# Kernel tuning notes

Measured on AMD Instinct MI355X. Metric: run time of the kernel, lower is better.

The kernel has to match this reference:

```python
import jax, jax.numpy as jnp
import numpy as np

B, S, D = 2, 2048, 1024
H, DH = 16, 64
INNER = H * DH  # 1024
FF = 4 * D
WINDOW = 128
EPS = 1e-5
SCALE = DH ** -0.5


def setup_inputs() -> dict:
    key = jax.random.key(0)
    ks = jax.random.split(key, 8)
    s = lambda fan_in: 1.0 / np.sqrt(fan_in)
    return {
        "x": jax.random.normal(ks[0], (B, S, D), dtype=jnp.float32),
        "ln1_g": jnp.ones((D,), jnp.float32),
        "ln1_b": jnp.zeros((D,), jnp.float32),
        "w_qkv": jax.random.uniform(ks[1], (3 * INNER, D), jnp.float32, -s(D), s(D)),
        "w_out": jax.random.uniform(ks[2], (D, INNER), jnp.float32, -s(INNER), s(INNER)),
        "b_out": jnp.zeros((D,), jnp.float32),
        "ln2_g": jnp.ones((D,), jnp.float32),
        "ln2_b": jnp.zeros((D,), jnp.float32),
        "w_ff1": jax.random.uniform(ks[3], (FF, D), jnp.float32, -s(D), s(D)),
        "b_ff1": jnp.zeros((FF,), jnp.float32),
        "w_ff2": jax.random.uniform(ks[4], (D, FF), jnp.float32, -s(FF), s(FF)),
        "b_ff2": jnp.zeros((D,), jnp.float32),
    }


def _layernorm(x, g, b):
    mu = jnp.mean(x, axis=-1, keepdims=True)
    var = jnp.mean(jnp.square(x - mu), axis=-1, keepdims=True)
    return (x - mu) * jax.lax.rsqrt(var + EPS) * g + b


def reference(x, ln1_g, ln1_b, w_qkv, w_out, b_out, ln2_g, ln2_b, w_ff1, b_ff1, w_ff2, b_ff2):
    # --- attention block ---
    residual = x
    h = _layernorm(x, ln1_g, ln1_b)
    qkv = h @ w_qkv.T                             # [B, S, 3*INNER]
    q, k, v = jnp.split(qkv, 3, axis=-1)
    reshape_heads = lambda t: t.reshape(B, S, H, DH).transpose(0, 2, 1, 3)  # [B,H,S,DH]
    q, k, v = map(reshape_heads, (q, k, v))
    q = q * SCALE
    scores = jnp.einsum("bhqd,bhkd->bhqk", q, k)  # dense [B,H,S,S]
    # local sparse pattern: attend iff |i-j| <= window_size
    idx = jnp.arange(S)
    local_mask = jnp.abs(idx[:, None] - idx[None, :]) <= WINDOW  # [S,S] bool
    scores = jnp.where(local_mask[None, None], scores, -jnp.inf)
    attn = jax.nn.softmax(scores, axis=-1)
    attn = jnp.nan_to_num(attn, nan=0.0)
    out = jnp.einsum("bhqk,bhkd->bhqd", attn, v)  # [B,H,S,DH]
    out = out.transpose(0, 2, 1, 3).reshape(B, S, INNER)
    out = out @ w_out.T + b_out                   # dropout inactive (eval)
    x = residual + out
    # --- FFN block ---
    residual = x
    h = _layernorm(x, ln2_g, ln2_b)
    h = jax.nn.gelu(h @ w_ff1.T + b_ff1, approximate=False)
    h = h @ w_ff2.T + b_ff2
    return residual + h
```

## Files before the change

### kernel.cpp

```cpp
#include <hip/hip_runtime.h>
#include <stdint.h>

#define SEQ    2048
#define NB     2
#define DMODEL 1024
#define NHEAD  16
#define HDIM   64
#define FFDIM  4096
#define WIN    128
#define MTOK   (NB*SEQ)

typedef short short8 __attribute__((ext_vector_type(8)));
typedef float f32x4  __attribute__((ext_vector_type(4)));

__device__ __forceinline__ float bf2f(uint16_t h){ return __uint_as_float(((uint32_t)h) << 16); }
__device__ __forceinline__ uint16_t f2bf(float f){
  uint32_t u = __float_as_uint(f);
  u += 0x7fffu + ((u >> 16) & 1u);
  return (uint16_t)(u >> 16);
}

__device__ __forceinline__ float gelu_f(float v){
  float u = 0.7978845608028654f * v * (1.0f + 0.044715f * v * v);
  u = fminf(fmaxf(u, -10.0f), 10.0f);
  const float e = __expf(2.0f * u);
  const float th = (e - 1.0f) / (e + 1.0f);
  return 0.5f * v * (1.0f + th);
}

__device__ __forceinline__ void gl_lds16(const void* g, void* l) {
  __builtin_amdgcn_global_load_lds((const __attribute__((address_space(1))) void*)g,
                                   (__attribute__((address_space(3))) void*)l, 16, 0, 0);
}

__global__ __launch_bounds__(256) void cvtln_kernel(
    const float* __restrict__ s0, const float* __restrict__ s1,
    const float* __restrict__ s2, const float* __restrict__ s3,
    uint16_t* __restrict__ d0, uint16_t* __restrict__ d1,
    uint16_t* __restrict__ d2, uint16_t* __restrict__ d3,
    const float* __restrict__ x, const float* __restrict__ g,
    const float* __restrict__ b, uint16_t* __restrict__ y)
{
  __shared__ float red[8];
  const int t = threadIdx.x;
  if (blockIdx.x < 12288) {
    size_t i = (size_t)blockIdx.x * 256 + t;
    const float* s; uint16_t* d; size_t off;
    if      (i <  768*1024) { s = s0; d = d0; off = i; }
    else if (i < 1024*1024) { s = s1; d = d1; off = i -  768*1024; }
    else if (i < 2048*1024) { s = s2; d = d2; off = i - 1024*1024; }
    else                    { s = s3; d = d3; off = i - 2048*1024; }
    const float4 v = ((const float4*)s)[off];
    uint2 o;
    o.x = (uint32_t)f2bf(v.x) | ((uint32_t)f2bf(v.y) << 16);
    o.y = (uint32_t)f2bf(v.z) | ((uint32_t)f2bf(v.w) << 16);
    ((uint2*)d)[off] = o;
  } else {
    const int row = blockIdx.x - 12288;
    const float4 v = ((const float4*)(x + (size_t)row * DMODEL))[t];
    float s1 = v.x + v.y + v.z + v.w;
    float s2 = v.x*v.x + v.y*v.y + v.z*v.z + v.w*v.w;
    #pragma unroll
    for (int off = 32; off; off >>= 1) { s1 += __shfl_xor(s1, off, 64); s2 += __shfl_xor(s2, off, 64); }
    const int w = t >> 6;
    if ((t & 63) == 0) { red[w] = s1; red[4+w] = s2; }
    __syncthreads();
    s1 = red[0]+red[1]+red[2]+red[3];
    s2 = red[4]+red[5]+red[6]+red[7];
    const float mu = s1 * (1.0f/DMODEL);
    const float var = s2 * (1.0f/DMODEL) - mu*mu;
    const float rs = rsqrtf(var + 1e-5f);
    const float4 gv = ((const float4*)g)[t];
    const float4 bv = ((const float4*)b)[t];
    uint2 o;
    o.x = (uint32_t)f2bf((v.x-mu)*rs*gv.x + bv.x) | ((uint32_t)f2bf((v.y-mu)*rs*gv.y + bv.y) << 16);
    o.y = (uint32_t)f2bf((v.z-mu)*rs*gv.z + bv.z) | ((uint32_t)f2bf((v.w-mu)*rs*gv.w + bv.w) << 16);
    ((uint2*)(y + (size_t)row * DMODEL))[t] = o;
  }
}

__global__ __launch_bounds__(256) void ln_kernel(const float* __restrict__ x,
                                                 const float* __restrict__ g,
                                                 const float* __restrict__ b,
                                                 uint16_t* __restrict__ y)
{
  const int row = blockIdx.x;
  const int t = threadIdx.x;
  const float4 v = ((const float4*)(x + (size_t)row * DMODEL))[t];
  float s1 = v.x + v.y + v.z + v.w;
  float s2 = v.x*v.x + v.y*v.y + v.z*v.z + v.w*v.w;
  #pragma unroll
  for (int off = 32; off; off >>= 1) { s1 += __shfl_xor(s1, off, 64); s2 += __shfl_xor(s2, off, 64); }
  __shared__ float red[8];
  const int w = t >> 6;
  if ((t & 63) == 0) { red[w] = s1; red[4+w] = s2; }
  __syncthreads();
  s1 = red[0]+red[1]+red[2]+red[3];
  s2 = red[4]+red[5]+red[6]+red[7];
  const float mu = s1 * (1.0f/DMODEL);
  const float var = s2 * (1.0f/DMODEL) - mu*mu;
  const float rs = rsqrtf(var + 1e-5f);
  const float4 gv = ((const float4*)g)[t];
  const float4 bv = ((const float4*)b)[t];
  uint2 o;
  o.x = (uint32_t)f2bf((v.x-mu)*rs*gv.x + bv.x) | ((uint32_t)f2bf((v.y-mu)*rs*gv.y + bv.y) << 16);
  o.y = (uint32_t)f2bf((v.z-mu)*rs*gv.z + bv.z) | ((uint32_t)f2bf((v.w-mu)*rs*gv.w + bv.w) << 16);
  ((uint2*)(y + (size_t)row * DMODEL))[t] = o;
}


template<int EPI>
__global__ __launch_bounds__(256) void gemm_bt(
    const uint16_t* __restrict__ A, const uint16_t* __restrict__ Bm,
    const float* __restrict__ bias, uint16_t* __restrict__ C,
    int M, int N, int K)
{
  __shared__ __align__(16) uint16_t As[128*64];
  __shared__ __align__(16) uint16_t Bs[128*64];
  const int t = threadIdx.x;
  const int l = t & 63;
  const int w = t >> 6;
  const int row0 = blockIdx.y * 128;
  const int col0 = blockIdx.x * 128;
  const int wm = (w >> 1) * 64, wn = (w & 1) * 64;

  f32x4 acc[4][4];
  #pragma unroll
  for (int i = 0; i < 4; ++i)
    #pragma unroll
    for (int j = 0; j < 4; ++j)
      #pragma unroll
      for (int e = 0; e < 4; ++e) acc[i][j][e] = 0.0f;

  const int sr8 = t >> 3;
  const int sg  = (t & 7) ^ (sr8 & 7);
  const uint16_t* aG = A  + (size_t)(row0 + sr8) * K + sg * 8;
  const uint16_t* bG = Bm + (size_t)(col0 + sr8) * K + sg * 8;
  char* aL = (char*)As + t * 16;
  char* bL = (char*)Bs + t * 16;
  const int mrow = l & 15;
  const int kq = l >> 4;

  for (int k0 = 0; k0 < K; k0 += 64) {
    #pragma unroll
    for (int c = 0; c < 4; ++c) {
      gl_lds16(aG + k0 + (size_t)(c*32) * K, aL + c*4096);
      gl_lds16(bG + k0 + (size_t)(c*32) * K, bL + c*4096);
    }
    __syncthreads();
    #pragma unroll
    for (int ks = 0; ks < 2; ++ks) {
      const int pa = ((ks*4 + kq) ^ (mrow & 7)) * 16;
      short8 af[4], bfr[4];
      #pragma unroll
      for (int mi = 0; mi < 4; ++mi)
        af[mi] = *(const short8*)((const char*)As + (wm + mi*16 + mrow) * 128 + pa);
      #pragma unroll
      for (int ni = 0; ni < 4; ++ni)
        bfr[ni] = *(const short8*)((const char*)Bs + (wn + ni*16 + mrow) * 128 + pa);
      #pragma unroll
      for (int mi = 0; mi < 4; ++mi)
        #pragma unroll
        for (int ni = 0; ni < 4; ++ni)
          acc[mi][ni] = __builtin_amdgcn_mfma_f32_16x16x32_bf16(af[mi], bfr[ni], acc[mi][ni], 0, 0, 0);
    }
    __syncthreads();
  }

  const int crow = (l >> 4) * 4;
  float bv[4];
  #pragma unroll
  for (int ni = 0; ni < 4; ++ni)
    bv[ni] = (EPI != 0) ? bias[col0 + wn + ni*16 + mrow] : 0.0f;
  #pragma unroll
  for (int mi = 0; mi < 4; ++mi) {
    #pragma unroll
    for (int r = 0; r < 4; ++r) {
      const int row = row0 + wm + mi*16 + crow + r;
      #pragma unroll
      for (int ni = 0; ni < 4; ++ni) {
        const int col = col0 + wn + ni*16 + mrow;
        float v = acc[mi][ni][r] + bv[ni];
        if (EPI == 2) v = gelu_f(v);
        C[(size_t)row * N + col] = f2bf(v);
      }
    }
  }
}

__global__ __launch_bounds__(256) void gemm_qkv(
    const uint16_t* __restrict__ A, const uint16_t* __restrict__ Bm,
    uint16_t* __restrict__ C, int M, int N, int K)
{
  __shared__ __align__(16) uint16_t As[128*64];
  __shared__ __align__(16) uint16_t Bs[64*64];
  const int t = threadIdx.x;
  const int l = t & 63;
  const int w = t >> 6;
  const int row0 = blockIdx.y * 128;
  const int col0 = blockIdx.x * 64;
  const int wm = (w >> 1) * 64, wn = (w & 1) * 32;

  f32x4 acc[4][2];
  #pragma unroll
  for (int i = 0; i < 4; ++i)
    #pragma unroll
    for (int j = 0; j < 2; ++j)
      #pragma unroll
      for (int e = 0; e < 4; ++e) acc[i][j][e] = 0.0f;

  const int sr8 = t >> 3;
  const int sg  = (t & 7) ^ (sr8 & 7);
  const uint16_t* aG = A  + (size_t)(row0 + sr8) * K + sg * 8;
  const uint16_t* bG = Bm + (size_t)(col0 + sr8) * K + sg * 8;
  char* aL = (char*)As + t * 16;
  char* bL = (char*)Bs + t * 16;
  const int mrow = l & 15;
  const int kq = l >> 4;

  for (int k0 = 0; k0 < K; k0 += 64) {
    #pragma unroll
    for (int c = 0; c < 4; ++c)
      gl_lds16(aG + k0 + (size_t)(c*32) * K, aL + c*4096);
    #pragma unroll
    for (int c = 0; c < 2; ++c)
      gl_lds16(bG + k0 + (size_t)(c*32) * K, bL + c*4096);
    __syncthreads();
    #pragma unroll
    for (int ks = 0; ks < 2; ++ks) {
      const int pa = ((ks*4 + kq) ^ (mrow & 7)) * 16;
      short8 af[4], bfr[2];
      #pragma unroll
      for (int mi = 0; mi < 4; ++mi)
        af[mi] = *(const short8*)((const char*)As + (wm + mi*16 + mrow) * 128 + pa);
      #pragma unroll
      for (int ni = 0; ni < 2; ++ni)
        bfr[ni] = *(const short8*)((const char*)Bs + (wn + ni*16 + mrow) * 128 + pa);
      #pragma unroll
      for (int mi = 0; mi < 4; ++mi)
        #pragma unroll
        for (int ni = 0; ni < 2; ++ni)
          acc[mi][ni] = __builtin_amdgcn_mfma_f32_16x16x32_bf16(af[mi], bfr[ni], acc[mi][ni], 0, 0, 0);
    }
    __syncthreads();
  }

  const int crow = (l >> 4) * 4;
  #pragma unroll
  for (int mi = 0; mi < 4; ++mi)
    #pragma unroll
    for (int r = 0; r < 4; ++r) {
      const int row = row0 + wm + mi*16 + crow + r;
      #pragma unroll
      for (int ni = 0; ni < 2; ++ni)
        C[(size_t)row * N + col0 + wn + ni*16 + mrow] = f2bf(acc[mi][ni][r]);
    }
}

__global__ __launch_bounds__(256) void gemm64(
    const uint16_t* __restrict__ A, const uint16_t* __restrict__ Bm,
    const float* __restrict__ bias, const float* __restrict__ res,
    float* __restrict__ out, int M, int N, int K)
{
  __shared__ __align__(16) uint16_t As[64*64];
  __shared__ __align__(16) uint16_t Bs[64*64];
  const int t = threadIdx.x;
  const int l = t & 63;
  const int w = t >> 6;
  const int row0 = blockIdx.y * 64;
  const int col0 = blockIdx.x * 64;
  const int wm = (w >> 1) * 32, wn = (w & 1) * 32;

  f32x4 acc[2][2];
  #pragma unroll
  for (int i = 0; i < 2; ++i)
    #pragma unroll
    for (int j = 0; j < 2; ++j)
      #pragma unroll
      for (int e = 0; e < 4; ++e) acc[i][j][e] = 0.0f;

  const int sr8 = t >> 3;
  const int sg  = (t & 7) ^ (sr8 & 7);
  const uint16_t* aG = A  + (size_t)(row0 + sr8) * K + sg * 8;
  const uint16_t* bG = Bm + (size_t)(col0 + sr8) * K + sg * 8;
  char* aL = (char*)As + t * 16;
  char* bL = (char*)Bs + t * 16;
  const int mrow = l & 15;
  const int kq = l >> 4;

  for (int k0 = 0; k0 < K; k0 += 64) {
    gl_lds16(aG + k0,                    aL);
    gl_lds16(aG + k0 + (size_t)32 * K,   aL + 4096);
    gl_lds16(bG + k0,                    bL);
    gl_lds16(bG + k0 + (size_t)32 * K,   bL + 4096);
    __syncthreads();
    #pragma unroll
    for (int ks = 0; ks < 2; ++ks) {
      const int pa = ((ks*4 + kq) ^ (mrow & 7)) * 16;
      short8 af[2], bfr[2];
      #pragma unroll
      for (int mi = 0; mi < 2; ++mi)
        af[mi] = *(const short8*)((const char*)As + (wm + mi*16 + mrow) * 128 + pa);
      #pragma unroll
      for (int ni = 0; ni < 2; ++ni)
        bfr[ni] = *(const short8*)((const char*)Bs + (wn + ni*16 + mrow) * 128 + pa);
      #pragma unroll
      for (int mi = 0; mi < 2; ++mi)
        #pragma unroll
        for (int ni = 0; ni < 2; ++ni)
          acc[mi][ni] = __builtin_amdgcn_mfma_f32_16x16x32_bf16(af[mi], bfr[ni], acc[mi][ni], 0, 0, 0);
    }
    __syncthreads();
  }

  const int crow = (l >> 4) * 4;
  float bv[2];
  #pragma unroll
  for (int ni = 0; ni < 2; ++ni)
    bv[ni] = bias[col0 + wn + ni*16 + mrow];
  #pragma unroll
  for (int mi = 0; mi < 2; ++mi)
    #pragma unroll
    for (int r = 0; r < 4; ++r) {
      const int row = row0 + wm + mi*16 + crow + r;
      #pragma unroll
      for (int ni = 0; ni < 2; ++ni) {
        const int col = col0 + wn + ni*16 + mrow;
        out[(size_t)row * N + col] = acc[mi][ni][r] + bv[ni] + res[(size_t)row * N + col];
      }
    }
}

#define TQ    32
#define NKT   18
#define NKP   (NKT*16)
#define KSTR  72
#define PSTR  296

__global__ __launch_bounds__(256) void attn_kernel(const uint16_t* __restrict__ qkv,
                                                   uint16_t* __restrict__ out)
{
  __shared__ uint16_t Qs[TQ * KSTR];
  __shared__ uint16_t Ps[TQ * PSTR];
  __shared__ uint16_t KV[NKP * KSTR];
  const int t = threadIdx.x, l = t & 63, w = t >> 6;
  const int b = blockIdx.z, hh = blockIdx.y, q0 = blockIdx.x * TQ;
  const int k0 = (q0 - WIN > 0) ? (q0 - WIN) : 0;
  const int kend_ = q0 + TQ + WIN;
  const int kend = (kend_ < SEQ) ? kend_ : SEQ;
  const int nk = kend - k0;

  {
    const int r = t >> 3, gg = t & 7;
    const uint4 qv = *(const uint4*)(qkv + (size_t)(b*SEQ + q0 + r) * 3072 + hh*64 + gg*8);
    *(uint4*)((char*)Qs + r*(KSTR*2) + gg*16) = qv;
    for (int j = r; j < NKP; j += 32) {
      uint4 kv; kv.x = 0; kv.y = 0; kv.z = 0; kv.w = 0;
      if (j < nk)
        kv = *(const uint4*)(qkv + (size_t)(b*SEQ + k0 + j) * 3072 + 1024 + hh*64 + gg*8);
      *(uint4*)((char*)KV + j*(KSTR*2) + gg*16) = kv;
    }
  }
  __syncthreads();

  if (w < 2) {
    const int rb = w * 16;
    const int mrow = l & 15, q4 = l >> 4;
    const short8 aq0 = *(const short8*)((const char*)Qs + (rb + mrow)*(KSTR*2) + q4*16);
    const short8 aq1 = *(const short8*)((const char*)Qs + (rb + mrow)*(KSTR*2) + 64 + q4*16);
    f32x4 cacc[NKT];
    #pragma unroll
    for (int ct = 0; ct < NKT; ++ct) {
      f32x4 c; c[0]=0.f; c[1]=0.f; c[2]=0.f; c[3]=0.f;
      const short8 b0 = *(const short8*)((const char*)KV + (ct*16 + mrow)*(KSTR*2) + q4*16);
      const short8 b1 = *(const short8*)((const char*)KV + (ct*16 + mrow)*(KSTR*2) + 64 + q4*16);
      c = __builtin_amdgcn_mfma_f32_16x16x32_bf16(aq0, b0, c, 0, 0, 0);
      c = __builtin_amdgcn_mfma_f32_16x16x32_bf16(aq1, b1, c, 0, 0, 0);
      cacc[ct] = c;
    }
    #pragma unroll
    for (int r = 0; r < 4; ++r) {
      const int iq = q0 + rb + q4*4 + r;
      float m = -1e30f;
      #pragma unroll
      for (int ct = 0; ct < NKT; ++ct) {
        const int jj = ct*16 + mrow;
        const int j = k0 + jj;
        const bool ok = (jj < nk) && (j >= iq - WIN) && (j <= iq + WIN);
        const float s = ok ? cacc[ct][r] * 0.125f : -1e30f;
        cacc[ct][r] = s;
        m = fmaxf(m, s);
      }
      m = fmaxf(m, __shfl_xor(m, 1, 64));
      m = fmaxf(m, __shfl_xor(m, 2, 64));
      m = fmaxf(m, __shfl_xor(m, 4, 64));
      m = fmaxf(m, __shfl_xor(m, 8, 64));
      float s = 0.f;
      #pragma unroll
      for (int ct = 0; ct < NKT; ++ct) {
        const float e = __expf(cacc[ct][r] - m);
        cacc[ct][r] = e;
        s += e;
      }
      s += __shfl_xor(s, 1, 64);
      s += __shfl_xor(s, 2, 64);
      s += __shfl_xor(s, 4, 64);
      s += __shfl_xor(s, 8, 64);
      const float rinv = 1.0f / s;
      #pragma unroll
      for (int ct = 0; ct < NKT; ++ct)
        Ps[(rb + q4*4 + r) * PSTR + ct*16 + mrow] = f2bf(cacc[ct][r] * rinv);
    }
  }
  __syncthreads();

  {
    uint16_t* Vt = KV;
    const int gg = t & 7;
    for (int j = t >> 3; j < NKP; j += 32) {
      if (j < nk) {
        const uint4 v = *(const uint4*)(qkv + (size_t)(b*SEQ + k0 + j) * 3072 + 2048 + hh*64 + gg*8);
        uint16_t e[8] = { (uint16_t)(v.x & 0xffff), (uint16_t)(v.x >> 16),
                          (uint16_t)(v.y & 0xffff), (uint16_t)(v.y >> 16),
                          (uint16_t)(v.z & 0xffff), (uint16_t)(v.z >> 16),
                          (uint16_t)(v.w & 0xffff), (uint16_t)(v.w >> 16) };
        #pragma unroll
        for (int dd = 0; dd < 8; ++dd) Vt[(gg*8 + dd) * PSTR + j] = e[dd];
      } else {
        #pragma unroll
        for (int dd = 0; dd < 8; ++dd) Vt[(gg*8 + dd) * PSTR + j] = 0;
      }
    }
  }
  __syncthreads();

  {
    const uint16_t* Vt = KV;
    const int mrow = l & 15, q4 = l >> 4;
    const int rt = w & 1, dt0 = (w >> 1) * 2;
    f32x4 o0, o1;
    #pragma unroll
    for (int e = 0; e < 4; ++e) { o0[e] = 0.f; o1[e] = 0.f; }
    #pragma unroll
    for (int ks = 0; ks < 9; ++ks) {
      const short8 a  = *(const short8*)((const char*)Ps + (rt*16 + mrow)*(PSTR*2) + ks*64 + q4*16);
      const short8 v0 = *(const short8*)((const char*)Vt + ((dt0  )*16 + mrow)*(PSTR*2) + ks*64 + q4*16);
      const short8 v1 = *(const short8*)((const char*)Vt + ((dt0+1)*16 + mrow)*(PSTR*2) + ks*64 + q4*16);
      o0 = __builtin_amdgcn_mfma_f32_16x16x32_bf16(a, v0, o0, 0, 0, 0);
      o1 = __builtin_amdgcn_mfma_f32_16x16x32_bf16(a, v1, o1, 0, 0, 0);
    }
    #pragma unroll
    for (int r = 0; r < 4; ++r) {
      const int iq = q0 + rt*16 + q4*4 + r;
      const size_t rowoff = (size_t)(b*SEQ + iq) * DMODEL + hh*64;
      out[rowoff + (dt0  )*16 + mrow] = f2bf(o0[r]);
      out[rowoff + (dt0+1)*16 + mrow] = f2bf(o1[r]);
    }
  }
}

extern "C" void kernel_launch(void* const* d_in, const int* in_sizes, int n_in,
                              void* d_out, int out_size, void* d_ws, size_t ws_size,
                              hipStream_t stream)
{
  const float* x    = (const float*)d_in[0];
  const float* ln1g = (const float*)d_in[1];
  const float* ln1b = (const float*)d_in[2];
  const float* wqkv = (const float*)d_in[3];
  const float* wout = (const float*)d_in[4];
  const float* bout = (const float*)d_in[5];
  const float* ln2g = (const float*)d_in[6];
  const float* ln2b = (const float*)d_in[7];
  const float* wff1 = (const float*)d_in[8];
  const float* bff1 = (const float*)d_in[9];
  const float* wff2 = (const float*)d_in[10];
  const float* bff2 = (const float*)d_in[11];
  float* out = (float*)d_out;

  char* ws = (char*)d_ws;
  const size_t MB = (size_t)1 << 20;
  uint16_t* Wqkv = (uint16_t*)(ws);
  uint16_t* Wout = (uint16_t*)(ws +  6*MB);
  uint16_t* Wff1 = (uint16_t*)(ws +  8*MB);
  uint16_t* Wff2 = (uint16_t*)(ws + 16*MB);
  uint16_t* QKV  = (uint16_t*)(ws + 24*MB);
  uint16_t* H1   = (uint16_t*)(ws + 48*MB);
  uint16_t* AT   = H1;
  float*    X2f  = (float*)   (ws + 56*MB);
  uint16_t* H2   = (uint16_t*)(ws + 72*MB);
  uint16_t* FF1  = (uint16_t*)(ws + 24*MB);

  cvtln_kernel<<<16384, 256, 0, stream>>>(wqkv, wout, wff1, wff2,
                                          Wqkv, Wout, Wff1, Wff2,
                                          x, ln1g, ln1b, H1);
  gemm_qkv<<<dim3(3072/64, MTOK/128), 256, 0, stream>>>(H1, Wqkv, QKV, MTOK, 3072, DMODEL);
  attn_kernel<<<dim3(SEQ/TQ, NHEAD, NB), 256, 0, stream>>>(QKV, AT);
  gemm64<<<dim3(DMODEL/64, MTOK/64), 256, 0, stream>>>(AT, Wout, bout, x, X2f, MTOK, DMODEL, DMODEL);
  ln_kernel<<<MTOK, 256, 0, stream>>>(X2f, ln2g, ln2b, H2);
  gemm_bt<2><<<dim3(FFDIM/128, MTOK/128), 256, 0, stream>>>(H2, Wff1, bff1, FF1, MTOK, FFDIM, DMODEL);
  gemm64<<<dim3(DMODEL/64, MTOK/64), 256, 0, stream>>>(FF1, Wff2, bff2, X2f, out, MTOK, DMODEL, FFDIM);
}
```

Before: 342.5 us.

## Replace QKV and FF1 GEMMs with 256x256 multi-stage pipelined kernel

```diff
diff --git a/kernel.cpp b/kernel.cpp
--- a/kernel.cpp
+++ b/kernel.cpp
@@ -31,6 +31,12 @@
 __device__ __forceinline__ void gl_lds16(const void* g, void* l) {
   __builtin_amdgcn_global_load_lds((const __attribute__((address_space(1))) void*)g,
                                    (__attribute__((address_space(3))) void*)l, 16, 0, 0);
+}
+
+__device__ __forceinline__ void BAR() {
+  asm volatile("" ::: "memory");
+  __builtin_amdgcn_s_barrier();
+  asm volatile("" ::: "memory");
 }
 
 __global__ __launch_bounds__(256) void cvtln_kernel(
@@ -108,153 +114,114 @@
   ((uint2*)(y + (size_t)row * DMODEL))[t] = o;
 }
 
-
 template<int EPI>
-__global__ __launch_bounds__(256) void gemm_bt(
+__global__ __launch_bounds__(512, 2) void gemm256(
     const uint16_t* __restrict__ A, const uint16_t* __restrict__ Bm,
     const float* __restrict__ bias, uint16_t* __restrict__ C,
     int M, int N, int K)
 {
-  __shared__ __align__(16) uint16_t As[128*64];
-  __shared__ __align__(16) uint16_t Bs[128*64];
+  __shared__ __align__(16) uint16_t L[4 * 16384];
   const int t = threadIdx.x;
   const int l = t & 63;
   const int w = t >> 6;
-  const int row0 = blockIdx.y * 128;
-  const int col0 = blockIdx.x * 128;
-  const int wm = (w >> 1) * 64, wn = (w & 1) * 64;
-
-  f32x4 acc[4][4];
-  #pragma unroll
-  for (int i = 0; i < 4; ++i)
+  const int wm = w >> 2, wn = w & 3;
+  const int row0 = blockIdx.y * 256, col0 = blockIdx.x * 256;
+  const int mrow = l & 15, kq = l >> 4;
+  const int nt = K >> 5;
+
+  f32x4 acc[8][4];
+  #pragma unroll
+  for (int i = 0; i < 8; ++i)
     #pragma unroll
     for (int j = 0; j < 4; ++j)
       #pragma unroll
       for (int e = 0; e < 4; ++e) acc[i][j][e] = 0.0f;
 
-  const int sr8 = t >> 3;
-  const int sg  = (t & 7) ^ (sr8 & 7);
-  const uint16_t* aG = A  + (size_t)(row0 + sr8) * K + sg * 8;
-  const uint16_t* bG = Bm + (size_t)(col0 + sr8) * K + sg * 8;
-  char* aL = (char*)As + t * 16;
-  char* bL = (char*)Bs + t * 16;
-  const int mrow = l & 15;
-  const int kq = l >> 4;
-
-  for (int k0 = 0; k0 < K; k0 += 64) {
-    #pragma unroll
-    for (int c = 0; c < 4; ++c) {
-      gl_lds16(aG + k0 + (size_t)(c*32) * K, aL + c*4096);
-      gl_lds16(bG + k0 + (size_t)(c*32) * K, bL + c*4096);
-    }
-    __syncthreads();
-    #pragma unroll
-    for (int ks = 0; ks < 2; ++ks) {
-      const int pa = ((ks*4 + kq) ^ (mrow & 7)) * 16;
-      short8 af[4], bfr[4];
-      #pragma unroll
-      for (int mi = 0; mi < 4; ++mi)
-        af[mi] = *(const short8*)((const char*)As + (wm + mi*16 + mrow) * 128 + pa);
+  const int sr = t >> 2;
+  const int kl = (t & 3) ^ ((t >> 3) & 3);
+  const uint16_t* aG = A  + (size_t)(row0 + sr) * K + kl * 8;
+  const uint16_t* bG = Bm + (size_t)(col0 + sr) * K + kl * 8;
+  char* const lds = (char*)L;
+  const int soff = t * 16;
+
+  #define STAGE_A(tt_) { char* d_ = lds + ((tt_) & 3) * 32768 + soff; \
+      gl_lds16(aG + (tt_) * 32, d_); \
+      gl_lds16(aG + (size_t)128 * K + (tt_) * 32, d_ + 8192); }
+  #define STAGE_B(tt_) { char* d_ = lds + ((tt_) & 3) * 32768 + 16384 + soff; \
+      gl_lds16(bG + (tt_) * 32, d_); \
+      gl_lds16(bG + (size_t)128 * K + (tt_) * 32, d_ + 8192); }
+
+  STAGE_A(0); STAGE_B(0);
+  STAGE_A(1); STAGE_B(1);
+  STAGE_A(2); STAGE_B(2);
+  asm volatile("s_waitcnt vmcnt(8)" ::: "memory");
+  BAR();
+
+  const int cphys = (kq ^ ((mrow >> 1) & 3)) << 4;
+
+  for (int tt = 0; tt < nt; ++tt) {
+    char* const bufA = lds + (tt & 3) * 32768;
+    char* const bufB = bufA + 16384;
+    short8 bf[4], af[4];
+    #pragma unroll
+    for (int ni = 0; ni < 4; ++ni)
+      bf[ni] = *(const short8*)(bufB + (wn*64 + ni*16 + mrow) * 64 + cphys);
+    #pragma unroll
+    for (int mi = 0; mi < 4; ++mi)
+      af[mi] = *(const short8*)(bufA + (wm*128 + mi*16 + mrow) * 64 + cphys);
+    if (tt + 3 < nt) STAGE_A(tt + 3);
+    BAR();
+    __builtin_amdgcn_s_setprio(1);
+    #pragma unroll
+    for (int mi = 0; mi < 4; ++mi)
       #pragma unroll
       for (int ni = 0; ni < 4; ++ni)
-        bfr[ni] = *(const short8*)((const char*)Bs + (wn + ni*16 + mrow) * 128 + pa);
-      #pragma unroll
-      for (int mi = 0; mi < 4; ++mi)
-        #pragma unroll
-        for (int ni = 0; ni < 4; ++ni)
-          acc[mi][ni] = __builtin_amdgcn_mfma_f32_16x16x32_bf16(af[mi], bfr[ni], acc[mi][ni], 0, 0, 0);
-    }
-    __syncthreads();
-  }
-
-  const int crow = (l >> 4) * 4;
+        acc[mi][ni] = __builtin_amdgcn_mfma_f32_16x16x32_bf16(af[mi], bf[ni], acc[mi][ni], 0, 0, 0);
+    __builtin_amdgcn_s_setprio(0);
+    BAR();
+    #pragma unroll
+    for (int mi = 0; mi < 4; ++mi)
+      af[mi] = *(const short8*)(bufA + (wm*128 + (mi+4)*16 + mrow) * 64 + cphys);
+    if (tt + 3 < nt) {
+      STAGE_B(tt + 3);
+      asm volatile("s_waitcnt vmcnt(8)" ::: "memory");
+    } else if (tt + 3 == nt) {
+      asm volatile("s_waitcnt vmcnt(4)" ::: "memory");
+    } else if (tt + 2 == nt) {
+      asm volatile("s_waitcnt vmcnt(0)" ::: "memory");
+    }
+    BAR();
+    __builtin_amdgcn_s_setprio(1);
+    #pragma unroll
+    for (int mi = 0; mi < 4; ++mi)
+      #pragma unroll
+      for (int ni = 0; ni < 4; ++ni)
+        acc[mi+4][ni] = __builtin_amdgcn_mfma_f32_16x16x32_bf16(af[mi], bf[ni], acc[mi+4][ni], 0, 0, 0);
+    __builtin_amdgcn_s_setprio(0);
+    BAR();
+  }
+  #undef STAGE_A
+  #undef STAGE_B
+
+  const int crow = kq * 4;
   float bv[4];
   #pragma unroll
   for (int ni = 0; ni < 4; ++ni)
-    bv[ni] = (EPI != 0) ? bias[col0 + wn + ni*16 + mrow] : 0.0f;
-  #pragma unroll
-  for (int mi = 0; mi < 4; ++mi) {
+    bv[ni] = (EPI != 0) ? bias[col0 + wn*64 + ni*16 + mrow] : 0.0f;
+  #pragma unroll
+  for (int mi = 0; mi < 8; ++mi) {
     #pragma unroll
     for (int r = 0; r < 4; ++r) {
-      const int row = row0 + wm + mi*16 + crow + r;
+      const int row = row0 + wm*128 + mi*16 + crow + r;
+      uint16_t* Cr = C + (size_t)row * N + col0 + wn*64 + mrow;
       #pragma unroll
       for (int ni = 0; ni < 4; ++ni) {
-        const int col = col0 + wn + ni*16 + mrow;
         float v = acc[mi][ni][r] + bv[ni];
         if (EPI == 2) v = gelu_f(v);
-        C[(size_t)row * N + col] = f2bf(v);
+        Cr[ni*16] = f2bf(v);
       }
     }
   }
-}
-
-__global__ __launch_bounds__(256) void gemm_qkv(
-    const uint16_t* __restrict__ A, const uint16_t* __restrict__ Bm,
-    uint16_t* __restrict__ C, int M, int N, int K)
-{
-  __shared__ __align__(16) uint16_t As[128*64];
-  __shared__ __align__(16) uint16_t Bs[64*64];
-  const int t = threadIdx.x;
-  const int l = t & 63;
-  const int w = t >> 6;
-  const int row0 = blockIdx.y * 128;
-  const int col0 = blockIdx.x * 64;
-  const int wm = (w >> 1) * 64, wn = (w & 1) * 32;
-
-  f32x4 acc[4][2];
-  #pragma unroll
-  for (int i = 0; i < 4; ++i)
-    #pragma unroll
-    for (int j = 0; j < 2; ++j)
-      #pragma unroll
-      for (int e = 0; e < 4; ++e) acc[i][j][e] = 0.0f;
-
-  const int sr8 = t >> 3;
-  const int sg  = (t & 7) ^ (sr8 & 7);
-  const uint16_t* aG = A  + (size_t)(row0 + sr8) * K + sg * 8;
-  const uint16_t* bG = Bm + (size_t)(col0 + sr8) * K + sg * 8;
-  char* aL = (char*)As + t * 16;
-  char* bL = (char*)Bs + t * 16;
-  const int mrow = l & 15;
-  const int kq = l >> 4;
-
-  for (int k0 = 0; k0 < K; k0 += 64) {
-    #pragma unroll
-    for (int c = 0; c < 4; ++c)
-      gl_lds16(aG + k0 + (size_t)(c*32) * K, aL + c*4096);
-    #pragma unroll
-    for (int c = 0; c < 2; ++c)
-      gl_lds16(bG + k0 + (size_t)(c*32) * K, bL + c*4096);
-    __syncthreads();
-    #pragma unroll
-    for (int ks = 0; ks < 2; ++ks) {
-      const int pa = ((ks*4 + kq) ^ (mrow & 7)) * 16;
-      short8 af[4], bfr[2];
-      #pragma unroll
-      for (int mi = 0; mi < 4; ++mi)
-        af[mi] = *(const short8*)((const char*)As + (wm + mi*16 + mrow) * 128 + pa);
-      #pragma unroll
-      for (int ni = 0; ni < 2; ++ni)
-        bfr[ni] = *(const short8*)((const char*)Bs + (wn + ni*16 + mrow) * 128 + pa);
-      #pragma unroll
-      for (int mi = 0; mi < 4; ++mi)
-        #pragma unroll
-        for (int ni = 0; ni < 2; ++ni)
-          acc[mi][ni] = __builtin_amdgcn_mfma_f32_16x16x32_bf16(af[mi], bfr[ni], acc[mi][ni], 0, 0, 0);
-    }
-    __syncthreads();
-  }
-
-  const int crow = (l >> 4) * 4;
-  #pragma unroll
-  for (int mi = 0; mi < 4; ++mi)
-    #pragma unroll
-    for (int r = 0; r < 4; ++r) {
-      const int row = row0 + wm + mi*16 + crow + r;
-      #pragma unroll
-      for (int ni = 0; ni < 2; ++ni)
-        C[(size_t)row * N + col0 + wn + ni*16 + mrow] = f2bf(acc[mi][ni][r]);
-    }
 }
 
 __global__ __launch_bounds__(256) void gemm64(
@@ -493,10 +460,10 @@
   cvtln_kernel<<<16384, 256, 0, stream>>>(wqkv, wout, wff1, wff2,
                                           Wqkv, Wout, Wff1, Wff2,
                                           x, ln1g, ln1b, H1);
-  gemm_qkv<<<dim3(3072/64, MTOK/128), 256, 0, stream>>>(H1, Wqkv, QKV, MTOK, 3072, DMODEL);
+  gemm256<0><<<dim3(3072/256, MTOK/256), 512, 0, stream>>>(H1, Wqkv, nullptr, QKV, MTOK, 3072, DMODEL);
   attn_kernel<<<dim3(SEQ/TQ, NHEAD, NB), 256, 0, stream>>>(QKV, AT);
   gemm64<<<dim3(DMODEL/64, MTOK/64), 256, 0, stream>>>(AT, Wout, bout, x, X2f, MTOK, DMODEL, DMODEL);
   ln_kernel<<<MTOK, 256, 0, stream>>>(X2f, ln2g, ln2b, H2);
-  gemm_bt<2><<<dim3(FFDIM/128, MTOK/128), 256, 0, stream>>>(H2, Wff1, bff1, FF1, MTOK, FFDIM, DMODEL);
+  gemm256<2><<<dim3(FFDIM/256, MTOK/256), 512, 0, stream>>>(H2, Wff1, bff1, FF1, MTOK, FFDIM, DMODEL);
   gemm64<<<dim3(DMODEL/64, MTOK/64), 256, 0, stream>>>(FF1, Wff2, bff2, X2f, out, MTOK, DMODEL, FFDIM);
 }
```

Measured after the change: 331.7 us. -3.2%, faster.
